# Optimization experiments

Measured on AMD Instinct MI355X. Metric: run time of the kernel, lower is better.

## Reference

```python
import jax, jax.numpy as jnp
import numpy as np

B, T, H = 2, 2048, 2048
E, K, I = 8, 2, 1408


def setup_inputs() -> dict:
    key = jax.random.key(0)
    ks = jax.random.split(key, 6)
    x = jax.random.normal(ks[0], (B, T, H), dtype=jnp.float32)
    # router: small-std, row-normalized init (as in the torch module)
    gw = jax.random.normal(ks[1], (E, H), dtype=jnp.float32) * 1e-3
    gw = gw / (jnp.linalg.norm(gw, axis=-1, keepdims=True) + 1e-6)
    scale1 = 1.0 / np.sqrt(H)
    scale2 = 1.0 / np.sqrt(I)
    W1 = jax.random.normal(ks[2], (E, H, I), dtype=jnp.float32) * scale1  # fc1 per expert
    W2 = jax.random.normal(ks[3], (E, I, H), dtype=jnp.float32) * scale2  # fc2 per expert
    Ws1 = jax.random.normal(ks[4], (H, I), dtype=jnp.float32) * scale1    # shared expert fc1
    Ws2 = jax.random.normal(ks[5], (I, H), dtype=jnp.float32) * scale2    # shared expert fc2
    return {"x": x, "gate_w": gw, "W1": W1, "W2": W2, "Ws1": Ws1, "Ws2": Ws2}


def reference(x, gate_w, W1, W2, Ws1, Ws2):
    b, t, h = x.shape
    nt = b * t
    x_flat = x.reshape(nt, h)

    # router
    gate_logits = x_flat @ gate_w.T                       # [nt, E]
    gate_probs = jax.nn.softmax(gate_logits.astype(jnp.float32), axis=-1)
    topk_vals, topk_idx = jax.lax.top_k(gate_probs, K)    # [nt, K]

    # aux (load-balancing) loss
    importance = gate_probs.mean(axis=0)                  # [E]
    load = jnp.zeros((E,), jnp.float32).at[topk_idx.reshape(-1)].add(1.0)
    load = load / (nt * K)
    aux_loss = (importance * load).sum() * E

    # combine weights: zero except at top-k experts (NOT renormalized, matching forward)
    combine = jnp.sum(jax.nn.one_hot(topk_idx, E, dtype=jnp.float32)
                      * topk_vals[..., None], axis=1)     # [nt, E]

    # dense expert compute (equivalent to gather-expert-scatter with 0 weights elsewhere)
    h1 = jnp.einsum('th,ehi->tei', x_flat, W1)            # [nt, E, I]
    h1 = h1 * jax.nn.sigmoid(h1)                          # SiLU
    expert_out = jnp.einsum('tei,eih->teh', h1, W2)       # [nt, E, H]
    y_flat = jnp.einsum('teh,te->th', expert_out, combine)

    # shared expert (always on)
    hs = x_flat @ Ws1
    y_flat = y_flat + (hs * jax.nn.sigmoid(hs)) @ Ws2

    y = y_flat.reshape(b, t, h).astype(x.dtype)
    return y, aux_loss
```

## Files before the change

kernel.cpp:

```cpp
#include <hip/hip_runtime.h>
#include <hip/hip_bf16.h>

#define NT 4096
#define HD 2048
#define NE 8
#define TOPK 2
#define ID 1408
#define NG 9
#define BM 128
#define BN 64
#define BK 64
#define MT_MAX 104
#define NWG1 2288
#define NTW 6336

typedef unsigned short u16;
typedef unsigned int u32;
typedef unsigned long long u64;
typedef __attribute__((ext_vector_type(8))) short bf16x8;
typedef __attribute__((ext_vector_type(4))) float f32x4;

__device__ __forceinline__ u16 f2bf(float f) {
    u32 u = __builtin_bit_cast(u32, f);
    u += 0x7FFFu + ((u >> 16) & 1u);
    return (u16)(u >> 16);
}
__device__ __forceinline__ float bflo(u32 v) { return __builtin_bit_cast(float, v << 16); }
__device__ __forceinline__ float bfhi(u32 v) { return __builtin_bit_cast(float, v & 0xffff0000u); }

typedef __attribute__((address_space(1))) const void gas_void;
typedef __attribute__((address_space(3))) void las_void;
__device__ __forceinline__ void gl_lds16(const void* g, void* l) {
    __builtin_amdgcn_global_load_lds((gas_void*)(u64)g, (las_void*)(u32)(u64)l, 16, 0, 0);
}

__global__ void router_tw1_kernel(const float* __restrict__ x, const float* __restrict__ gw,
                                  int* __restrict__ counts, float* __restrict__ imp,
                                  int* __restrict__ tki, float* __restrict__ tkv,
                                  u16* __restrict__ xb,
                                  const float* __restrict__ W1, const float* __restrict__ Ws1,
                                  u16* __restrict__ wt1) {
    __shared__ float s_imp[NE];
    __shared__ int s_cnt[NE];
    __shared__ u16 Lt[64][68];
    int tid = threadIdx.x;
    if (blockIdx.x < NT / 4) {
        if (tid < NE) { s_imp[tid] = 0.f; s_cnt[tid] = 0; }
        int w = tid >> 6, lane = tid & 63;
        int t = blockIdx.x * 4 + w;
        float acc[NE];
#pragma unroll
        for (int e = 0; e < NE; e++) acc[e] = 0.f;
        const float* xr = x + (size_t)t * HD;
        u16* xw = xb + (size_t)t * HD;
#pragma unroll
        for (int i = 0; i < 4; i++) {
            int cc = i * 64 + lane;
            int b64 = cc >> 3, j = cc & 7, h = j >> 2, q = j & 3;
            int k0 = b64 * 64 + h * 32 + q * 4;
            float4 v0 = *(const float4*)(xr + k0);
            float4 v1 = *(const float4*)(xr + k0 + 16);
#pragma unroll
            for (int e = 0; e < NE; e++) {
                const float* gp = gw + e * HD + k0;
                float4 g0 = *(const float4*)(gp);
                float4 g1 = *(const float4*)(gp + 16);
                acc[e] += v0.x * g0.x + v0.y * g0.y + v0.z * g0.z + v0.w * g0.w
                        + v1.x * g1.x + v1.y * g1.y + v1.z * g1.z + v1.w * g1.w;
            }
            ushort4 o0, o1;
            o0.x = f2bf(v0.x); o0.y = f2bf(v0.y); o0.z = f2bf(v0.z); o0.w = f2bf(v0.w);
            o1.x = f2bf(v1.x); o1.y = f2bf(v1.y); o1.z = f2bf(v1.z); o1.w = f2bf(v1.w);
            uint4 o;
            o.x = (u32)o0.x | ((u32)o0.y << 16); o.y = (u32)o0.z | ((u32)o0.w << 16);
            o.z = (u32)o1.x | ((u32)o1.y << 16); o.w = (u32)o1.z | ((u32)o1.w << 16);
            *(uint4*)(xw + b64 * 64 + j * 8) = o;
        }
#pragma unroll
        for (int e = 0; e < NE; e++) {
#pragma unroll
            for (int o = 32; o >= 1; o >>= 1) acc[e] += __shfl_xor(acc[e], o, 64);
        }
        __syncthreads();
        if (lane == 0) {
            float mx = acc[0];
            for (int e = 1; e < NE; e++) mx = fmaxf(mx, acc[e]);
            float p[NE], sum = 0.f;
            for (int e = 0; e < NE; e++) { p[e] = expf(acc[e] - mx); sum += p[e]; }
            float inv = 1.f / sum;
            for (int e = 0; e < NE; e++) p[e] *= inv;
            int i1 = 0;
            for (int e = 1; e < NE; e++) if (p[e] > p[i1]) i1 = e;
            int i2 = (i1 == 0) ? 1 : 0;
            for (int e = 0; e < NE; e++) if (e != i1 && p[e] > p[i2]) i2 = e;
            tki[t * 2 + 0] = i1; tkv[t * 2 + 0] = p[i1];
            tki[t * 2 + 1] = i2; tkv[t * 2 + 1] = p[i2];
            for (int e = 0; e < NE; e++) atomicAdd(&s_imp[e], p[e]);
            atomicAdd(&s_cnt[i1], 1); atomicAdd(&s_cnt[i2], 1);
        }
        __syncthreads();
        if (tid < NE) {
            atomicAdd(&imp[tid], s_imp[tid]);
            atomicAdd(&counts[tid], s_cnt[tid]);
        }
    } else {
        int tw = blockIdx.x - NT / 4;
        int e = tw / 704, rem = tw % 704;
        int n0 = (rem % 22) * 64, k0 = (rem / 22) * 64;
        const float* src = (e < NE) ? (W1 + (size_t)e * HD * ID) : Ws1;
        u16* dst = wt1 + (size_t)e * ID * HD;
#pragma unroll
        for (int i = 0; i < 4; i++) {
            int idx = i * 256 + tid;
            int kl = idx >> 4, nq = (idx & 15) * 4;
            float4 v = *(const float4*)(src + (size_t)(k0 + kl) * ID + n0 + nq);
            Lt[nq + 0][kl] = f2bf(v.x); Lt[nq + 1][kl] = f2bf(v.y);
            Lt[nq + 2][kl] = f2bf(v.z); Lt[nq + 3][kl] = f2bf(v.w);
        }
        __syncthreads();
#pragma unroll
        for (int c2 = 0; c2 < 2; c2++) {
            int cid = tid * 2 + c2;
            int nr = cid >> 3, j = cid & 7;
            int h = j >> 2, q = j & 3;
            int kb = h * 32 + q * 4;
            uint2 lo = *(const uint2*)&Lt[nr][kb];
            uint2 hi = *(const uint2*)&Lt[nr][kb + 16];
            uint4 o; o.x = lo.x; o.y = lo.y; o.z = hi.x; o.w = hi.y;
            *(uint4*)(dst + (size_t)(n0 + nr) * HD + k0 + j * 8) = o;
        }
    }
}

__global__ void prepscat_kernel(const int* __restrict__ counts, const float* __restrict__ imp,
                                int* __restrict__ off, int* __restrict__ tileoff,
                                float* __restrict__ out_aux,
                                int* __restrict__ tki, const float* __restrict__ tkv,
                                int* __restrict__ list, float* __restrict__ wgt) {
    __shared__ int s_off[NG];
    __shared__ int s_cur[NE];
    int tid = threadIdx.x;
    if (tid == 0) {
        int o = 0, to = 0;
        for (int g = 0; g < NG; g++) {
            int c = (g < NE) ? counts[g] : NT;
            off[g] = o; s_off[g] = o; tileoff[g] = to;
            o += c; to += (c + BM - 1) / BM;
        }
        off[NG] = o; tileoff[NG] = to;
        float aux = 0.f;
        for (int e = 0; e < NE; e++)
            aux += (imp[e] / (float)NT) * ((float)counts[e] / (float)(NT * TOPK));
        *out_aux = aux * (float)NE;
    }
    if (tid < NE) s_cur[tid] = 0;
    __syncthreads();
    for (int t = tid; t < NT; t += 256) {
#pragma unroll
        for (int k = 0; k < TOPK; k++) {
            int e = tki[t * 2 + k];
            int pos = atomicAdd(&s_cur[e], 1);
            int s = s_off[e] + pos;
            list[s] = t;
            wgt[s] = tkv[t * 2 + k];
            tki[t * 2 + k] = s;
        }
        list[s_off[NE] + t] = t;
        wgt[s_off[NE] + t] = 1.0f;
    }
}

__global__ void transw_kernel(const float* __restrict__ W, const float* __restrict__ Wsh,
                              u16* __restrict__ dst, int K, int N) {
    int e = blockIdx.z;
    const float* src = (e < NE) ? (W + (size_t)e * K * N) : Wsh;
    dst += (size_t)e * N * K;
    int k0 = blockIdx.y * 64, n0 = blockIdx.x * 64;
    __shared__ u16 Lt[64][68];
    int tid = threadIdx.x;
#pragma unroll
    for (int i = 0; i < 4; i++) {
        int idx = i * 256 + tid;
        int kl = idx >> 4, nq = (idx & 15) * 4;
        float4 v = *(const float4*)(src + (size_t)(k0 + kl) * N + n0 + nq);
        Lt[nq + 0][kl] = f2bf(v.x); Lt[nq + 1][kl] = f2bf(v.y);
        Lt[nq + 2][kl] = f2bf(v.z); Lt[nq + 3][kl] = f2bf(v.w);
    }
    __syncthreads();
#pragma unroll
    for (int c2 = 0; c2 < 2; c2++) {
        int cid = tid * 2 + c2;
        int nr = cid >> 3, j = cid & 7;
        int h = j >> 2, q = j & 3;
        int kb = h * 32 + q * 4;
        uint2 lo = *(const uint2*)&Lt[nr][kb];
        uint2 hi = *(const uint2*)&Lt[nr][kb + 16];
        uint4 o; o.x = lo.x; o.y = lo.y; o.z = hi.x; o.w = hi.y;
        *(uint4*)(dst + (size_t)(n0 + nr) * K + k0 + j * 8) = o;
    }
}

template <bool FTW>
__global__ __launch_bounds__(256) void fc1_kernel(
    const u16* __restrict__ xb, const u16* __restrict__ Wt1,
    const int* __restrict__ off, const int* __restrict__ tileoff,
    const int* __restrict__ list, u16* __restrict__ h1,
    const float* __restrict__ W2, const float* __restrict__ Ws2,
    u16* __restrict__ wt2) {
    __shared__ u16 S[2 * 12288];
    int wg0 = blockIdx.x;
    int tid = threadIdx.x;
    if (FTW && wg0 >= NWG1) {
        u16 (*Lt)[68] = (u16(*)[68])S;
        int tw = wg0 - NWG1;
        int e = tw / 704, rem = tw % 704;
        int n0 = (rem % 32) * 64, k0 = (rem / 32) * 64;
        const float* src = (e < NE) ? (W2 + (size_t)e * ID * HD) : Ws2;
        u16* dst = wt2 + (size_t)e * HD * ID;
#pragma unroll
        for (int i = 0; i < 4; i++) {
            int idx = i * 256 + tid;
            int kl = idx >> 4, nq = (idx & 15) * 4;
            float4 v = *(const float4*)(src + (size_t)(k0 + kl) * HD + n0 + nq);
            Lt[nq + 0][kl] = f2bf(v.x); Lt[nq + 1][kl] = f2bf(v.y);
            Lt[nq + 2][kl] = f2bf(v.z); Lt[nq + 3][kl] = f2bf(v.w);
        }
        __syncthreads();
#pragma unroll
        for (int c2 = 0; c2 < 2; c2++) {
            int cid = tid * 2 + c2;
            int nr = cid >> 3, j = cid & 7;
            int h = j >> 2, q = j & 3;
            int kb = h * 32 + q * 4;
            uint2 lo = *(const uint2*)&Lt[nr][kb];
            uint2 hi = *(const uint2*)&Lt[nr][kb + 16];
            uint4 o; o.x = lo.x; o.y = lo.y; o.z = hi.x; o.w = hi.y;
            *(uint4*)(dst + (size_t)(n0 + nr) * ID + k0 + j * 8) = o;
        }
        return;
    }
    int orig = wg0;
    int wg = (orig & 7) * (NWG1 >> 3) + (orig >> 3);
    int bx = wg % (ID / BN), mt = wg / (ID / BN);

    int g = -1, gto = 0;
#pragma unroll
    for (int gg = 0; gg < NG; gg++)
        if (mt >= tileoff[gg] && mt < tileoff[gg + 1]) { g = gg; gto = tileoff[gg]; }
    if (g < 0) return;
    int goff = off[g], cnt = off[g + 1] - goff;
    int row0 = (mt - gto) * BM;
    const u16* Wb = Wt1 + (size_t)g * (ID * HD);
    int n0 = bx * BN;
    int lane = tid & 63, w = tid >> 6;
    int lm = lane >> 3;
    int lc = (((lane & 7) ^ lm) << 3);
    const u16* pa[4]; const u16* pb[2];
#pragma unroll
    for (int i = 0; i < 4; i++) {
        int c = i * 4 + w;
        int r = row0 + c * 8 + lm;
        r = (r < cnt) ? r : (cnt - 1);
        pa[i] = xb + (size_t)list[goff + r] * HD + lc;
    }
#pragma unroll
    for (int i = 0; i < 2; i++) {
        int c = i * 4 + w;
        pb[i] = Wb + (size_t)(n0 + c * 8 + lm) * HD + lc;
    }
    int wr = w >> 1, wc = w & 1;
    int lr = lane & 15, l7 = lane & 7, q2 = lane >> 4;
    f32x4 acc[4][2] = {};

    auto stage = [&](int b) {
        u16* A = S + b * 12288;
        u16* B = A + 8192;
#pragma unroll
        for (int i = 0; i < 4; i++) { gl_lds16(pa[i], A + (i * 4 + w) * 512); pa[i] += BK; }
#pragma unroll
        for (int i = 0; i < 2; i++) { gl_lds16(pb[i], B + (i * 4 + w) * 512); pb[i] += BK; }
    };
    auto compute = [&](int b) {
        const u16* A = S + b * 12288;
        const u16* B = A + 8192;
#pragma unroll
        for (int kc = 0; kc < 8; kc += 4) {
            int slot = ((kc + q2) ^ l7) << 3;
            bf16x8 a[4], bb[2];
#pragma unroll
            for (int f = 0; f < 4; f++)
                a[f] = __builtin_bit_cast(bf16x8, *(const uint4*)&A[(wr * 64 + f * 16 + lr) * BK + slot]);
#pragma unroll
            for (int f = 0; f < 2; f++)
                bb[f] = __builtin_bit_cast(bf16x8, *(const uint4*)&B[(wc * 32 + f * 16 + lr) * BK + slot]);
            __builtin_amdgcn_s_setprio(1);
#pragma unroll
            for (int mf = 0; mf < 4; mf++)
#pragma unroll
                for (int nf = 0; nf < 2; nf++)
                    acc[mf][nf] = __builtin_amdgcn_mfma_f32_16x16x32_bf16(a[mf], bb[nf], acc[mf][nf], 0, 0, 0);
            __builtin_amdgcn_s_setprio(0);
        }
    };

    stage(0);
    int cur = 0;
    for (int t = 1; t < HD / BK; ++t) {
        stage(cur ^ 1);
        asm volatile("s_waitcnt vmcnt(6)" ::: "memory");
        __builtin_amdgcn_s_barrier();
        compute(cur);
        asm volatile("s_waitcnt lgkmcnt(0)" ::: "memory");
        __builtin_amdgcn_s_barrier();
        cur ^= 1;
    }
    asm volatile("s_waitcnt vmcnt(0)" ::: "memory");
    __builtin_amdgcn_s_barrier();
    compute(cur);

    int q4 = q2 * 4;
    int cl = ((lr >> 2) << 3) + (lr & 3);
#pragma unroll
    for (int mf = 0; mf < 4; mf++)
#pragma unroll
        for (int reg = 0; reg < 4; reg++) {
            int r = row0 + wr * 64 + mf * 16 + q4 + reg;
            if (r < cnt) {
                size_t rb = (size_t)(goff + r) * ID + n0;
#pragma unroll
                for (int nf = 0; nf < 2; nf++) {
                    float v = acc[mf][nf][reg];
                    h1[rb + wc * 32 + (nf << 2) + cl] = f2bf(v / (1.f + __expf(-v)));
                }
            }
        }
}

template <bool EO>
__global__ __launch_bounds__(256) void fc2_kernel(
    const u16* __restrict__ h1, const u16* __restrict__ Wt2,
    const int* __restrict__ off, const int* __restrict__ tileoff,
    const int* __restrict__ list, const float* __restrict__ wgt,
    u16* __restrict__ eo, float* __restrict__ y) {
    __shared__ u16 S[2 * 12288];
    int nwg = gridDim.x * gridDim.y;
    int orig = blockIdx.y * gridDim.x + blockIdx.x;
    int wg = (orig & 7) * (nwg >> 3) + (orig >> 3);
    int bx = wg % gridDim.x, mt = wg / gridDim.x;

    int g = -1, gto = 0;
#pragma unroll
    for (int gg = 0; gg < NG; gg++)
        if (mt >= tileoff[gg] && mt < tileoff[gg + 1]) { g = gg; gto = tileoff[gg]; }
    if (g < 0) return;
    int goff = off[g], cnt = off[g + 1] - goff;
    int row0 = (mt - gto) * BM;
    const u16* Wb = Wt2 + (size_t)g * (ID * HD);
    int n0 = bx * BN;
    int tid = threadIdx.x, lane = tid & 63, w = tid >> 6;
    int lm = lane >> 3;
    int lc = (((lane & 7) ^ lm) << 3);
    const u16* pa[4]; const u16* pb[2];
#pragma unroll
    for (int i = 0; i < 4; i++) {
        int c = i * 4 + w;
        int r = row0 + c * 8 + lm;
        r = (r < cnt) ? r : (cnt - 1);
        pa[i] = h1 + (size_t)(goff + r) * ID + lc;
    }
#pragma unroll
    for (int i = 0; i < 2; i++) {
        int c = i * 4 + w;
        pb[i] = Wb + (size_t)(n0 + c * 8 + lm) * ID + lc;
    }
    int wr = w >> 1, wc = w & 1;
    int lr = lane & 15, l7 = lane & 7, q2 = lane >> 4;
    f32x4 acc[4][2] = {};

    auto stage = [&](int b) {
        u16* A = S + b * 12288;
        u16* B = A + 8192;
#pragma unroll
        for (int i = 0; i < 4; i++) { gl_lds16(pa[i], A + (i * 4 + w) * 512); pa[i] += BK; }
#pragma unroll
        for (int i = 0; i < 2; i++) { gl_lds16(pb[i], B + (i * 4 + w) * 512); pb[i] += BK; }
    };
    auto compute = [&](int b) {
        const u16* A = S + b * 12288;
        const u16* B = A + 8192;
#pragma unroll
        for (int kc = 0; kc < 8; kc += 4) {
            int slot = ((kc + q2) ^ l7) << 3;
            bf16x8 a[4], bb[2];
#pragma unroll
            for (int f = 0; f < 4; f++)
                a[f] = __builtin_bit_cast(bf16x8, *(const uint4*)&A[(wr * 64 + f * 16 + lr) * BK + slot]);
#pragma unroll
            for (int f = 0; f < 2; f++)
                bb[f] = __builtin_bit_cast(bf16x8, *(const uint4*)&B[(wc * 32 + f * 16 + lr) * BK + slot]);
            __builtin_amdgcn_s_setprio(1);
#pragma unroll
            for (int mf = 0; mf < 4; mf++)
#pragma unroll
                for (int nf = 0; nf < 2; nf++)
                    acc[mf][nf] = __builtin_amdgcn_mfma_f32_16x16x32_bf16(a[mf], bb[nf], acc[mf][nf], 0, 0, 0);
            __builtin_amdgcn_s_setprio(0);
        }
    };

    stage(0);
    int cur = 0;
    for (int t = 1; t < ID / BK; ++t) {
        stage(cur ^ 1);
        asm volatile("s_waitcnt vmcnt(6)" ::: "memory");
        __builtin_amdgcn_s_barrier();
        compute(cur);
        asm volatile("s_waitcnt lgkmcnt(0)" ::: "memory");
        __builtin_amdgcn_s_barrier();
        cur ^= 1;
    }
    asm volatile("s_waitcnt vmcnt(0)" ::: "memory");
    __builtin_amdgcn_s_barrier();
    compute(cur);

    int q4 = q2 * 4;
#pragma unroll
    for (int mf = 0; mf < 4; mf++)
#pragma unroll
        for (int reg = 0; reg < 4; reg++) {
            int r = row0 + wr * 64 + mf * 16 + q4 + reg;
            if (r < cnt) {
                int slot = goff + r;
                if (EO) {
                    size_t rb = (size_t)slot * HD + n0 + wc * 32;
#pragma unroll
                    for (int nf = 0; nf < 2; nf++)
                        eo[rb + nf * 16 + lr] = f2bf(acc[mf][nf][reg]);
                } else {
                    int tok = list[slot];
                    float wv = wgt[slot];
                    float* yr = y + (size_t)tok * HD + n0 + wc * 32;
#pragma unroll
                    for (int nf = 0; nf < 2; nf++)
                        atomicAdd(yr + nf * 16 + lr, acc[mf][nf][reg] * wv);
                }
            }
        }
}

__global__ __launch_bounds__(256) void combine_kernel(
    const u16* __restrict__ eo, const int* __restrict__ smap,
    const float* __restrict__ tkv, const int* __restrict__ off,
    float* __restrict__ y) {
    int idx = blockIdx.x * 256 + threadIdx.x;
    int t = idx >> 8;
    int cc = (idx & 255) << 3;
    int s0 = smap[t * 2 + 0], s1 = smap[t * 2 + 1];
    float w0 = tkv[t * 2 + 0], w1 = tkv[t * 2 + 1];
    int s2 = off[NE] + t;
    uint4 A = *(const uint4*)(eo + (size_t)s0 * HD + cc);
    uint4 B = *(const uint4*)(eo + (size_t)s1 * HD + cc);
    uint4 C = *(const uint4*)(eo + (size_t)s2 * HD + cc);
    float4 o0, o1;
    o0.x = w0 * bflo(A.x) + w1 * bflo(B.x) + bflo(C.x);
    o0.y = w0 * bfhi(A.x) + w1 * bfhi(B.x) + bfhi(C.x);
    o0.z = w0 * bflo(A.y) + w1 * bflo(B.y) + bflo(C.y);
    o0.w = w0 * bfhi(A.y) + w1 * bfhi(B.y) + bfhi(C.y);
    o1.x = w0 * bflo(A.z) + w1 * bflo(B.z) + bflo(C.z);
    o1.y = w0 * bfhi(A.z) + w1 * bfhi(B.z) + bfhi(C.z);
    o1.z = w0 * bflo(A.w) + w1 * bflo(B.w) + bflo(C.w);
    o1.w = w0 * bfhi(A.w) + w1 * bfhi(B.w) + bfhi(C.w);
    float* yr = y + (size_t)t * HD + cc;
    *(float4*)yr = o0;
    *(float4*)(yr + 4) = o1;
}

extern "C" void kernel_launch(void* const* d_in, const int* in_sizes, int n_in,
                              void* d_out, int out_size, void* d_ws, size_t ws_size,
                              hipStream_t stream) {
    const float* x   = (const float*)d_in[0];
    const float* gw  = (const float*)d_in[1];
    const float* W1  = (const float*)d_in[2];
    const float* W2  = (const float*)d_in[3];
    const float* Ws1 = (const float*)d_in[4];
    const float* Ws2 = (const float*)d_in[5];
    float* out = (float*)d_out;

    char* ws = (char*)d_ws;
    int*   counts  = (int*)(ws + 0);
    int*   off     = (int*)(ws + 128);
    int*   tileoff = (int*)(ws + 192);
    float* imp     = (float*)(ws + 256);
    int*   tki     = (int*)(ws + 320);
    float* tkv     = (float*)(ws + 33088);
    int*   list    = (int*)(ws + 65856);
    float* wgt     = (float*)(ws + 115008);
    u16* xb  = (u16*)(ws + 164352);
    u16* wt1 = (u16*)(ws + 16941568ULL);
    u16* h1  = (u16*)(ws + 68846080ULL);
    u16* eo  = (u16*)(ws + 103449088ULL);
    const bool use_big = (ws_size >= 205685248ULL);
    const bool use_eo  = (ws_size >= 153780736ULL);
    u16* wt2 = use_big ? (u16*)(ws + 153780736ULL) : (u16*)(ws + 164352);

    if (!use_eo)
        hipMemsetAsync(d_out, 0, (size_t)out_size * sizeof(float), stream);
    hipMemsetAsync(d_ws, 0, 320, stream);

    router_tw1_kernel<<<NT / 4 + NTW, 256, 0, stream>>>(
        x, gw, counts, imp, tki, tkv, xb, W1, Ws1, wt1);
    prepscat_kernel<<<1, 256, 0, stream>>>(
        counts, imp, off, tileoff, out + (size_t)NT * HD, tki, tkv, list, wgt);

    if (use_big) {
        fc1_kernel<true><<<NWG1 + NTW, 256, 0, stream>>>(
            xb, wt1, off, tileoff, list, h1, W2, Ws2, wt2);
    } else {
        fc1_kernel<false><<<NWG1, 256, 0, stream>>>(
            xb, wt1, off, tileoff, list, h1, W2, Ws2, wt2);
        transw_kernel<<<dim3(HD / 64, ID / 64, NG), 256, 0, stream>>>(W2, Ws2, wt2, ID, HD);
    }

    if (use_eo) {
        fc2_kernel<true><<<dim3(HD / BN, MT_MAX), 256, 0, stream>>>(
            h1, wt2, off, tileoff, list, wgt, eo, out);
        combine_kernel<<<NT, 256, 0, stream>>>(eo, tki, tkv, off, out);
    } else {
        fc2_kernel<false><<<dim3(HD / BN, MT_MAX), 256, 0, stream>>>(
            h1, wt2, off, tileoff, list, wgt, eo, out);
    }
}
```

Baseline: 305.4 us.

## Enlarge fc1/fc2 GEMM tiles to 128x128 with 512-thread workgroups

```diff
diff --git a/kernel.cpp b/kernel.cpp
--- a/kernel.cpp
+++ b/kernel.cpp
@@ -8,10 +8,10 @@
 #define ID 1408
 #define NG 9
 #define BM 128
-#define BN 64
+#define BN 128
 #define BK 64
 #define MT_MAX 104
-#define NWG1 2288
+#define NWG1 1144
 #define NTW 6336
 
 typedef unsigned short u16;
@@ -201,13 +201,13 @@
 }
 
 template <bool FTW>
-__global__ __launch_bounds__(256) void fc1_kernel(
+__global__ __launch_bounds__(512, 4) void fc1_kernel(
     const u16* __restrict__ xb, const u16* __restrict__ Wt1,
     const int* __restrict__ off, const int* __restrict__ tileoff,
     const int* __restrict__ list, u16* __restrict__ h1,
     const float* __restrict__ W2, const float* __restrict__ Ws2,
     u16* __restrict__ wt2) {
-    __shared__ u16 S[2 * 12288];
+    __shared__ u16 S[2 * 16384];
     int wg0 = blockIdx.x;
     int tid = threadIdx.x;
     if (FTW && wg0 >= NWG1) {
@@ -218,17 +218,16 @@
         const float* src = (e < NE) ? (W2 + (size_t)e * ID * HD) : Ws2;
         u16* dst = wt2 + (size_t)e * HD * ID;
 #pragma unroll
-        for (int i = 0; i < 4; i++) {
-            int idx = i * 256 + tid;
+        for (int i = 0; i < 2; i++) {
+            int idx = i * 512 + tid;
             int kl = idx >> 4, nq = (idx & 15) * 4;
             float4 v = *(const float4*)(src + (size_t)(k0 + kl) * HD + n0 + nq);
             Lt[nq + 0][kl] = f2bf(v.x); Lt[nq + 1][kl] = f2bf(v.y);
             Lt[nq + 2][kl] = f2bf(v.z); Lt[nq + 3][kl] = f2bf(v.w);
         }
         __syncthreads();
-#pragma unroll
-        for (int c2 = 0; c2 < 2; c2++) {
-            int cid = tid * 2 + c2;
+        {
+            int cid = tid;
             int nr = cid >> 3, j = cid & 7;
             int h = j >> 2, q = j & 3;
             int kb = h * 32 + q * 4;
@@ -239,8 +238,7 @@
         }
         return;
     }
-    int orig = wg0;
-    int wg = (orig & 7) * (NWG1 >> 3) + (orig >> 3);
+    int wg = (wg0 & 7) * (NWG1 >> 3) + (wg0 >> 3);
     int bx = wg % (ID / BN), mt = wg / (ID / BN);
 
     int g = -1, gto = 0;
@@ -253,35 +251,29 @@
     const u16* Wb = Wt1 + (size_t)g * (ID * HD);
     int n0 = bx * BN;
     int lane = tid & 63, w = tid >> 6;
-    int lm = lane >> 3;
-    int lc = (((lane & 7) ^ lm) << 3);
-    const u16* pa[4]; const u16* pb[2];
-#pragma unroll
-    for (int i = 0; i < 4; i++) {
-        int c = i * 4 + w;
-        int r = row0 + c * 8 + lm;
-        r = (r < cnt) ? r : (cnt - 1);
-        pa[i] = xb + (size_t)list[goff + r] * HD + lc;
-    }
-#pragma unroll
-    for (int i = 0; i < 2; i++) {
-        int c = i * 4 + w;
-        pb[i] = Wb + (size_t)(n0 + c * 8 + lm) * HD + lc;
-    }
-    int wr = w >> 1, wc = w & 1;
+    int r0 = tid >> 3, r1 = 64 + r0;
+    int lc = (((tid & 7) ^ (r0 & 7)) << 3);
+    int ra0 = row0 + r0; ra0 = (ra0 < cnt) ? ra0 : (cnt - 1);
+    int ra1 = row0 + r1; ra1 = (ra1 < cnt) ? ra1 : (cnt - 1);
+    const u16* pa0 = xb + (size_t)list[goff + ra0] * HD + lc;
+    const u16* pa1 = xb + (size_t)list[goff + ra1] * HD + lc;
+    const u16* pb0 = Wb + (size_t)(n0 + r0) * HD + lc;
+    const u16* pb1 = Wb + (size_t)(n0 + r1) * HD + lc;
+
+    int wr = w >> 2, wc = w & 3;
     int lr = lane & 15, l7 = lane & 7, q2 = lane >> 4;
     f32x4 acc[4][2] = {};
 
     auto stage = [&](int b) {
-        u16* A = S + b * 12288;
+        u16* A = S + b * 16384;
         u16* B = A + 8192;
-#pragma unroll
-        for (int i = 0; i < 4; i++) { gl_lds16(pa[i], A + (i * 4 + w) * 512); pa[i] += BK; }
-#pragma unroll
-        for (int i = 0; i < 2; i++) { gl_lds16(pb[i], B + (i * 4 + w) * 512); pb[i] += BK; }
+        gl_lds16(pa0, A + tid * 8);        pa0 += BK;
+        gl_lds16(pa1, A + 4096 + tid * 8); pa1 += BK;
+        gl_lds16(pb0, B + tid * 8);        pb0 += BK;
+        gl_lds16(pb1, B + 4096 + tid * 8); pb1 += BK;
     };
     auto compute = [&](int b) {
-        const u16* A = S + b * 12288;
+        const u16* A = S + b * 16384;
         const u16* B = A + 8192;
 #pragma unroll
         for (int kc = 0; kc < 8; kc += 4) {
@@ -307,7 +299,7 @@
     int cur = 0;
     for (int t = 1; t < HD / BK; ++t) {
         stage(cur ^ 1);
-        asm volatile("s_waitcnt vmcnt(6)" ::: "memory");
+        asm volatile("s_waitcnt vmcnt(4)" ::: "memory");
         __builtin_amdgcn_s_barrier();
         compute(cur);
         asm volatile("s_waitcnt lgkmcnt(0)" ::: "memory");
@@ -337,12 +329,12 @@
 }
 
 template <bool EO>
-__global__ __launch_bounds__(256) void fc2_kernel(
+__global__ __launch_bounds__(512, 4) void fc2_kernel(
     const u16* __restrict__ h1, const u16* __restrict__ Wt2,
     const int* __restrict__ off, const int* __restrict__ tileoff,
     const int* __restrict__ list, const float* __restrict__ wgt,
     u16* __restrict__ eo, float* __restrict__ y) {
-    __shared__ u16 S[2 * 12288];
+    __shared__ u16 S[2 * 16384];
     int nwg = gridDim.x * gridDim.y;
     int orig = blockIdx.y * gridDim.x + blockIdx.x;
     int wg = (orig & 7) * (nwg >> 3) + (orig >> 3);
@@ -358,35 +350,29 @@
     const u16* Wb = Wt2 + (size_t)g * (ID * HD);
     int n0 = bx * BN;
     int tid = threadIdx.x, lane = tid & 63, w = tid >> 6;
-    int lm = lane >> 3;
-    int lc = (((lane & 7) ^ lm) << 3);
-    const u16* pa[4]; const u16* pb[2];
-#pragma unroll
-    for (int i = 0; i < 4; i++) {
-        int c = i * 4 + w;
-        int r = row0 + c * 8 + lm;
-        r = (r < cnt) ? r : (cnt - 1);
-        pa[i] = h1 + (size_t)(goff + r) * ID + lc;
-    }
-#pragma unroll
-    for (int i = 0; i < 2; i++) {
-        int c = i * 4 + w;
-        pb[i] = Wb + (size_t)(n0 + c * 8 + lm) * ID + lc;
-    }
-    int wr = w >> 1, wc = w & 1;
+    int r0 = tid >> 3, r1 = 64 + r0;
+    int lc = (((tid & 7) ^ (r0 & 7)) << 3);
+    int ra0 = row0 + r0; ra0 = (ra0 < cnt) ? ra0 : (cnt - 1);
+    int ra1 = row0 + r1; ra1 = (ra1 < cnt) ? ra1 : (cnt - 1);
+    const u16* pa0 = h1 + (size_t)(goff + ra0) * ID + lc;
+    const u16* pa1 = h1 + (size_t)(goff + ra1) * ID + lc;
+    const u16* pb0 = Wb + (size_t)(n0 + r0) * ID + lc;
+    const u16* pb1 = Wb + (size_t)(n0 + r1) * ID + lc;
+
+    int wr = w >> 2, wc = w & 3;
     int lr = lane & 15, l7 = lane & 7, q2 = lane >> 4;
     f32x4 acc[4][2] = {};
 
     auto stage = [&](int b) {
-        u16* A = S + b * 12288;
+        u16* A = S + b * 16384;
         u16* B = A + 8192;
-#pragma unroll
-        for (int i = 0; i < 4; i++) { gl_lds16(pa[i], A + (i * 4 + w) * 512); pa[i] += BK; }
-#pragma unroll
-        for (int i = 0; i < 2; i++) { gl_lds16(pb[i], B + (i * 4 + w) * 512); pb[i] += BK; }
+        gl_lds16(pa0, A + tid * 8);        pa0 += BK;
+        gl_lds16(pa1, A + 4096 + tid * 8); pa1 += BK;
+        gl_lds16(pb0, B + tid * 8);        pb0 += BK;
+        gl_lds16(pb1, B + 4096 + tid * 8); pb1 += BK;
     };
     auto compute = [&](int b) {
-        const u16* A = S + b * 12288;
+        const u16* A = S + b * 16384;
         const u16* B = A + 8192;
 #pragma unroll
         for (int kc = 0; kc < 8; kc += 4) {
@@ -412,7 +398,7 @@
     int cur = 0;
     for (int t = 1; t < ID / BK; ++t) {
         stage(cur ^ 1);
-        asm volatile("s_waitcnt vmcnt(6)" ::: "memory");
+        asm volatile("s_waitcnt vmcnt(4)" ::: "memory");
         __builtin_amdgcn_s_barrier();
         compute(cur);
         asm volatile("s_waitcnt lgkmcnt(0)" ::: "memory");
@@ -513,20 +499,20 @@
         counts, imp, off, tileoff, out + (size_t)NT * HD, tki, tkv, list, wgt);
 
     if (use_big) {
-        fc1_kernel<true><<<NWG1 + NTW, 256, 0, stream>>>(
+        fc1_kernel<true><<<NWG1 + NTW, 512, 0, stream>>>(
             xb, wt1, off, tileoff, list, h1, W2, Ws2, wt2);
     } else {
-        fc1_kernel<false><<<NWG1, 256, 0, stream>>>(
+        fc1_kernel<false><<<NWG1, 512, 0, stream>>>(
             xb, wt1, off, tileoff, list, h1, W2, Ws2, wt2);
         transw_kernel<<<dim3(HD / 64, ID / 64, NG), 256, 0, stream>>>(W2, Ws2, wt2, ID, HD);
     }
 
     if (use_eo) {
-        fc2_kernel<true><<<dim3(HD / BN, MT_MAX), 256, 0, stream>>>(
+        fc2_kernel<true><<<dim3(HD / BN, MT_MAX), 512, 0, stream>>>(
             h1, wt2, off, tileoff, list, wgt, eo, out);
         combine_kernel<<<NT, 256, 0, stream>>>(eo, tki, tkv, off, out);
     } else {
-        fc2_kernel<false><<<dim3(HD / BN, MT_MAX), 256, 0, stream>>>(
+        fc2_kernel<false><<<dim3(HD / BN, MT_MAX), 512, 0, stream>>>(
             h1, wt2, off, tileoff, list, wgt, eo, out);
     }
 }
```

After: 272.4 us. -10.8%, faster.
